# Optimization experiments

Measured on AMD Instinct MI355X. Metric: run time of the kernel, lower is better.

## Reference

```python
import jax, jax.numpy as jnp
import numpy as np

SNUM = 8           # number of select-PUF stages
PUF_LEN = 64       # arbiter PUF length -> phi dim = PUF_LEN + 1
BATCH = 262144     # number of challenge-response pairs
D = 2 ** SNUM      # 256 combinations


def _make_kron_tables():
    """Replicates the W/B kron construction from combineMPUF.__init__.
    Returns Wmat, Bmat of shape [SNUM, D]; row i is W[i]/B[i] (originally [1, D])."""
    tmpX = np.array([[1], [1]])
    Ws, Bs = [], []
    for i in range(SNUM):
        w = np.array([[-1], [1]])
        b = np.array([[1], [0]])
        for _ in range(i + 1, SNUM):
            w = np.kron(tmpX, w)
            b = np.kron(tmpX, b)
        for _ in range(i):
            w = np.kron(w, tmpX)
            b = np.kron(b, tmpX)
        Ws.append(w.T[0])
        Bs.append(b.T[0])
    return (jnp.asarray(np.stack(Ws), jnp.float32),
            jnp.asarray(np.stack(Bs), jnp.float32))


def setup_inputs() -> dict:
    key = jax.random.key(0)
    k_phi, k_ws, k_bs, k_wd, k_bd = jax.random.split(key, 5)
    F = PUF_LEN + 1
    scale = 1.0 / np.sqrt(F)  # ~ torch Linear init scale
    phi = jax.random.normal(k_phi, (BATCH, F), dtype=jnp.float32)
    W_S = jax.random.uniform(k_ws, (SNUM, F), jnp.float32, -scale, scale)
    b_S = jax.random.uniform(k_bs, (SNUM,), jnp.float32, -scale, scale)
    W_D = jax.random.uniform(k_wd, (D, F), jnp.float32, -scale, scale)
    b_D = jax.random.uniform(k_bd, (D,), jnp.float32, -scale, scale)
    Wmat, Bmat = _make_kron_tables()
    return {"phi": phi, "W_S": W_S, "b_S": b_S, "W_D": W_D, "b_D": b_D,
            "Wmat": Wmat, "Bmat": Bmat}


def reference(phi, W_S, b_S, W_D, b_D, Wmat, Bmat):
    # phi: [B, F]; W_S: [SNUM, F]; W_D: [D, F]; Wmat/Bmat: [SNUM, D]
    Sdelta = phi @ W_S.T + b_S            # [B, SNUM]
    Ddelta = phi @ W_D.T + b_D            # [B, D]
    Souts = jax.nn.sigmoid(Sdelta)        # [B, SNUM]
    Douts = jax.nn.sigmoid(Ddelta)        # [B, D]
    # sigmoid-gated outer-product chain: M = prod_i (s_i * w_i + b_i)
    M = jnp.ones_like(Douts)
    for i in range(SNUM):                 # small fixed structural loop
        M = M * (Souts[:, i:i + 1] * Wmat[i] + Bmat[i])
    ans = jnp.sum(Douts * M * 0.99999, axis=-1, keepdims=True)  # [B, 1]
    reliability_output = jnp.abs(Sdelta)  # [B, SNUM]
    return ans, reliability_output
```

## Files before the change

### kernel.cpp

```cpp
#include <hip/hip_runtime.h>

typedef float  f32x4  __attribute__((ext_vector_type(4)));
typedef float  f32x4a __attribute__((ext_vector_type(4), aligned(4)));
typedef __bf16 bf16x8 __attribute__((ext_vector_type(8)));
typedef short  short8 __attribute__((ext_vector_type(8)));

#define F      65
#define NTT    17
#define KS3    3
#define RPB    128
#define NEGL2E -1.4426950408889634f

__device__ __forceinline__ float fast_sigmoid(float x) {
  float e = __builtin_amdgcn_exp2f(NEGL2E * x);
  return __builtin_amdgcn_rcpf(1.0f + e);
}
__device__ __forceinline__ float sig_prescaled(float a) {
  return __builtin_amdgcn_rcpf(1.0f + __builtin_amdgcn_exp2f(a));
}
template<int CTRL>
__device__ __forceinline__ float dpp_mov(float v) {
  return __builtin_bit_cast(float,
    __builtin_amdgcn_update_dpp(0, __builtin_bit_cast(int, v), CTRL, 0xF, 0xF, true));
}
__device__ __forceinline__ float reduce16(float v) {
  v += dpp_mov<0xB1>(v);
  v += dpp_mov<0x4E>(v);
  v += dpp_mov<0x141>(v);
  v += dpp_mov<0x140>(v);
  return v;
}

__global__ void prep_w(const float* __restrict__ W_S, const float* __restrict__ b_S,
                       const float* __restrict__ W_D, const float* __restrict__ b_D,
                       unsigned short* __restrict__ wsb) {
  int b = blockIdx.x;
  int t = b / 3, s = b % 3;
  int l = threadIdx.x;
  int c = l & 15, q = l >> 4;
  short8 out;
#pragma unroll
  for (int j = 0; j < 8; ++j) {
    int k = 32 * s + 8 * q + j;
    float v = 0.0f;
    if (t < 16) {
      int n = 16 * t + c;
      if (k < F)       v = NEGL2E * W_D[n * F + k];
      else if (k == F) v = NEGL2E * b_D[n];
    } else if (c < 8) {
      if (k < F)       v = W_S[c * F + k];
      else if (k == F) v = b_S[c];
    }
    unsigned int u = __builtin_bit_cast(unsigned int, v);
    u += 0x7FFFu + ((u >> 16) & 1u);
    out[j] = (short)(u >> 16);
  }
  reinterpret_cast<short8*>(wsb)[b * 64 + l] = out;
}

__launch_bounds__(256, 6)
__global__ void mpuf_main(const float* __restrict__ phi,
                          const unsigned short* __restrict__ wsb,
                          float* __restrict__ out_ans,
                          float* __restrict__ out_rel) {
  __shared__ float soutv[RPB][12];
  __shared__ float mtT[16][132];
  __shared__ float mlT[16][132];
  __shared__ float relv[RPB][8];

  const int tid  = threadIdx.x;
  const int wave = tid >> 6;
  const int l    = tid & 63;
  const int c    = l & 15;
  const int q    = l >> 4;
  const int wrow = wave * 32;
  const int R0b  = wrow + q * 4;
  const int brow = blockIdx.x * RPB;
  const int tbase = blockIdx.x & 15;

  const float* prow0 = phi + (size_t)(brow + wrow + c) * F;
  const float* prow1 = prow0 + (size_t)16 * F;

  f32x4a f40[4], f41[4];
#pragma unroll
  for (int s = 0; s < 2; ++s) {
    f40[2 * s]     = *reinterpret_cast<const f32x4a*>(prow0 + 32 * s + 8 * q);
    f40[2 * s + 1] = *reinterpret_cast<const f32x4a*>(prow0 + 32 * s + 8 * q + 4);
    f41[2 * s]     = *reinterpret_cast<const f32x4a*>(prow1 + 32 * s + 8 * q);
    f41[2 * s + 1] = *reinterpret_cast<const f32x4a*>(prow1 + 32 * s + 8 * q + 4);
  }
  const float a640 = prow0[64];
  const float a641 = prow1[64];

  const short8* wsv = reinterpret_cast<const short8*>(wsb);
  short8 bcur[3], bnxt[3];
#pragma unroll
  for (int s = 0; s < 3; ++s) bcur[s] = wsv[(16 * KS3 + s) * 64 + l];
#pragma unroll
  for (int s = 0; s < 3; ++s) bnxt[s] = wsv[(tbase * KS3 + s) * 64 + l];

  bf16x8 af0[3], af1[3];
#pragma unroll
  for (int s = 0; s < 2; ++s) {
    bf16x8 v0, v1;
#pragma unroll
    for (int j = 0; j < 4; ++j) {
      v0[j]     = (__bf16)f40[s * 2][j];
      v0[j + 4] = (__bf16)f40[s * 2 + 1][j];
      v1[j]     = (__bf16)f41[s * 2][j];
      v1[j + 4] = (__bf16)f41[s * 2 + 1][j];
    }
    af0[s] = v0; af1[s] = v1;
  }
  {
    bf16x8 v0 = {}, v1 = {};
    if (q == 0) {
      v0[0] = (__bf16)a640; v0[1] = (__bf16)1.0f;
      v1[0] = (__bf16)a641; v1[1] = (__bf16)1.0f;
    }
    af0[2] = v0; af1[2] = v1;
  }

  f32x4 aS0 = {}, aS1 = {};
#pragma unroll
  for (int s = 0; s < KS3; ++s) {
    bf16x8 b = __builtin_bit_cast(bf16x8, bcur[s]);
    aS0 = __builtin_amdgcn_mfma_f32_16x16x32_bf16(af0[s], b, aS0, 0, 0, 0);
    aS1 = __builtin_amdgcn_mfma_f32_16x16x32_bf16(af1[s], b, aS1, 0, 0, 0);
  }
  if (c < 8) {
#pragma unroll
    for (int r = 0; r < 4; ++r) {
      const int R0 = R0b + r, R1 = R0 + 16;
      relv[R0][c]  = fabsf(aS0[r]);
      relv[R1][c]  = fabsf(aS1[r]);
      soutv[R0][c] = fast_sigmoid(aS0[r]);
      soutv[R1][c] = fast_sigmoid(aS1[r]);
    }
  }

  {
    const int row = l >> 1, half = l & 1;
    f32x4 v = *reinterpret_cast<const f32x4*>(&relv[wrow + row][half * 4]);
    *reinterpret_cast<f32x4*>(
        &out_rel[(size_t)(brow + wrow + row) * 8 + half * 4]) = v;
  }

#pragma unroll
  for (int rr = 0; rr < 8; ++rr) {
    const int R = wrow + (rr & 4) * 4 + q * 4 + (rr & 3);
    f32x4 s03 = *reinterpret_cast<const f32x4*>(&soutv[R][0]);
    f32x4 s47 = *reinterpret_cast<const f32x4*>(&soutv[R][4]);
    float m = 0.99999f;
    m *= (c & 1) ? s03[0] : 1.0f - s03[0];
    m *= (c & 2) ? s03[1] : 1.0f - s03[1];
    m *= (c & 4) ? s03[2] : 1.0f - s03[2];
    m *= (c & 8) ? s03[3] : 1.0f - s03[3];
    mlT[c][R] = m;
    float mt = (c & 1) ? s47[0] : 1.0f - s47[0];
    mt *= (c & 2) ? s47[1] : 1.0f - s47[1];
    mt *= (c & 4) ? s47[2] : 1.0f - s47[2];
    mt *= (c & 8) ? s47[3] : 1.0f - s47[3];
    mtT[c][R] = mt;
  }

  float ans0[4] = {0, 0, 0, 0}, ans1[4] = {0, 0, 0, 0};

#pragma unroll 1
  for (int tt = 0; tt < 16; ++tt) {
    const int t  = (tt + tbase) & 15;
    const int tn = (tt + 1 + tbase) & 15;
    short8 bt[3];
#pragma unroll
    for (int s = 0; s < 3; ++s) bt[s] = bnxt[s];
#pragma unroll
    for (int s = 0; s < 3; ++s)
      bnxt[s] = wsv[(tn * KS3 + s) * 64 + l];
    f32x4 w0 = *reinterpret_cast<const f32x4*>(&mtT[t][R0b]);
    f32x4 w1 = *reinterpret_cast<const f32x4*>(&mtT[t][R0b + 16]);
    f32x4 A0 = {}, A1 = {};
#pragma unroll
    for (int s = 0; s < KS3; ++s) {
      bf16x8 b = __builtin_bit_cast(bf16x8, bt[s]);
      A0 = __builtin_amdgcn_mfma_f32_16x16x32_bf16(af0[s], b, A0, 0, 0, 0);
      A1 = __builtin_amdgcn_mfma_f32_16x16x32_bf16(af1[s], b, A1, 0, 0, 0);
    }
#pragma unroll
    for (int r = 0; r < 4; ++r) {
      ans0[r] = fmaf(sig_prescaled(A0[r]), w0[r], ans0[r]);
      ans1[r] = fmaf(sig_prescaled(A1[r]), w1[r], ans1[r]);
    }
  }

  f32x4 ml0 = *reinterpret_cast<const f32x4*>(&mlT[c][R0b]);
  f32x4 ml1 = *reinterpret_cast<const f32x4*>(&mlT[c][R0b + 16]);
  f32x4 o0, o1;
#pragma unroll
  for (int r = 0; r < 4; ++r) {
    o0[r] = reduce16(ml0[r] * ans0[r]);
    o1[r] = reduce16(ml1[r] * ans1[r]);
  }
  if (c == 0) {
    *reinterpret_cast<f32x4*>(&out_ans[brow + wrow + q * 4])      = o0;
    *reinterpret_cast<f32x4*>(&out_ans[brow + wrow + 16 + q * 4]) = o1;
  }
}

extern "C" void kernel_launch(void* const* d_in, const int* in_sizes, int n_in,
                              void* d_out, int out_size, void* d_ws, size_t ws_size,
                              hipStream_t stream) {
  const float* phi = (const float*)d_in[0];
  const float* W_S = (const float*)d_in[1];
  const float* b_S = (const float*)d_in[2];
  const float* W_D = (const float*)d_in[3];
  const float* b_D = (const float*)d_in[4];
  const int rows = in_sizes[0] / F;
  unsigned short* wsb = (unsigned short*)d_ws;
  float* out_ans = (float*)d_out;
  float* out_rel = out_ans + rows;
  hipLaunchKernelGGL(prep_w, dim3(NTT * KS3), dim3(64), 0, stream,
                     W_S, b_S, W_D, b_D, wsb);
  hipLaunchKernelGGL(mpuf_main, dim3(rows / RPB), dim3(256), 0, stream,
                     phi, wsb, out_ans, out_rel);
}
```

Before: 37.25 us.

## Stage packed weights in LDS and double rows per block

Each 512-thread block now copies the whole packed bf16 weight table (about 52 KB) into shared memory once. The MFMA loops then read weight fragments from LDS instead of issuing per-wave global loads, and the per-block tile-rotation offset is dropped. The block size doubles to 256 rows. The low-half mask products stay in registers instead of going through a shared array, and the reliability staging buffer reuses the mtT storage. In exchange, the large LDS footprint and the extra barrier limit how many blocks fit per CU, and every block pays the cost of filling the table before any compute starts.

```diff
diff --git a/kernel.cpp b/kernel.cpp
--- a/kernel.cpp
+++ b/kernel.cpp
@@ -8,7 +8,8 @@
 #define F      65
 #define NTT    17
 #define KS3    3
-#define RPB    128
+#define RPB    256
+#define NCHUNK (NTT*KS3*64)
 #define NEGL2E -1.4426950408889634f
 
 __device__ __forceinline__ float fast_sigmoid(float x) {
@@ -58,15 +59,14 @@
   reinterpret_cast<short8*>(wsb)[b * 64 + l] = out;
 }
 
-__launch_bounds__(256, 6)
+__launch_bounds__(512, 4)
 __global__ void mpuf_main(const float* __restrict__ phi,
                           const unsigned short* __restrict__ wsb,
                           float* __restrict__ out_ans,
                           float* __restrict__ out_rel) {
-  __shared__ float soutv[RPB][12];
-  __shared__ float mtT[16][132];
-  __shared__ float mlT[16][132];
-  __shared__ float relv[RPB][8];
+  __shared__ short8 ldsB[NCHUNK];
+  __shared__ float  soutv[RPB][12];
+  __shared__ float  mtT[16][260];
 
   const int tid  = threadIdx.x;
   const int wave = tid >> 6;
@@ -76,7 +76,8 @@
   const int wrow = wave * 32;
   const int R0b  = wrow + q * 4;
   const int brow = blockIdx.x * RPB;
-  const int tbase = blockIdx.x & 15;
+
+  float* relbuf = &mtT[0][0];
 
   const float* prow0 = phi + (size_t)(brow + wrow + c) * F;
   const float* prow1 = prow0 + (size_t)16 * F;
@@ -93,11 +94,11 @@
   const float a641 = prow1[64];
 
   const short8* wsv = reinterpret_cast<const short8*>(wsb);
-  short8 bcur[3], bnxt[3];
-#pragma unroll
-  for (int s = 0; s < 3; ++s) bcur[s] = wsv[(16 * KS3 + s) * 64 + l];
-#pragma unroll
-  for (int s = 0; s < 3; ++s) bnxt[s] = wsv[(tbase * KS3 + s) * 64 + l];
+#pragma unroll
+  for (int i = 0; i < 7; ++i) {
+    int idx = tid + i * 512;
+    if (idx < NCHUNK) ldsB[idx] = wsv[idx];
+  }
 
   bf16x8 af0[3], af1[3];
 #pragma unroll
@@ -121,19 +122,26 @@
     af0[2] = v0; af1[2] = v1;
   }
 
+  __syncthreads();
+
   f32x4 aS0 = {}, aS1 = {};
 #pragma unroll
   for (int s = 0; s < KS3; ++s) {
-    bf16x8 b = __builtin_bit_cast(bf16x8, bcur[s]);
+    bf16x8 b = __builtin_bit_cast(bf16x8, ldsB[(16 * KS3 + s) * 64 + l]);
     aS0 = __builtin_amdgcn_mfma_f32_16x16x32_bf16(af0[s], b, aS0, 0, 0, 0);
     aS1 = __builtin_amdgcn_mfma_f32_16x16x32_bf16(af1[s], b, aS1, 0, 0, 0);
   }
+
+  short8 bnxt[3];
+#pragma unroll
+  for (int s = 0; s < 3; ++s) bnxt[s] = ldsB[s * 64 + l];
+
   if (c < 8) {
 #pragma unroll
     for (int r = 0; r < 4; ++r) {
       const int R0 = R0b + r, R1 = R0 + 16;
-      relv[R0][c]  = fabsf(aS0[r]);
-      relv[R1][c]  = fabsf(aS1[r]);
+      relbuf[R0 * 8 + c] = fabsf(aS0[r]);
+      relbuf[R1 * 8 + c] = fabsf(aS1[r]);
       soutv[R0][c] = fast_sigmoid(aS0[r]);
       soutv[R1][c] = fast_sigmoid(aS1[r]);
     }
@@ -141,11 +149,14 @@
 
   {
     const int row = l >> 1, half = l & 1;
-    f32x4 v = *reinterpret_cast<const f32x4*>(&relv[wrow + row][half * 4]);
+    f32x4 v = *reinterpret_cast<const f32x4*>(&relbuf[(wrow + row) * 8 + half * 4]);
     *reinterpret_cast<f32x4*>(
         &out_rel[(size_t)(brow + wrow + row) * 8 + half * 4]) = v;
   }
 
+  __syncthreads();
+
+  float Ml0[4], Ml1[4];
 #pragma unroll
   for (int rr = 0; rr < 8; ++rr) {
     const int R = wrow + (rr & 4) * 4 + q * 4 + (rr & 3);
@@ -156,7 +167,7 @@
     m *= (c & 2) ? s03[1] : 1.0f - s03[1];
     m *= (c & 4) ? s03[2] : 1.0f - s03[2];
     m *= (c & 8) ? s03[3] : 1.0f - s03[3];
-    mlT[c][R] = m;
+    if (rr < 4) Ml0[rr & 3] = m; else Ml1[rr & 3] = m;
     float mt = (c & 1) ? s47[0] : 1.0f - s47[0];
     mt *= (c & 2) ? s47[1] : 1.0f - s47[1];
     mt *= (c & 4) ? s47[2] : 1.0f - s47[2];
@@ -167,15 +178,14 @@
   float ans0[4] = {0, 0, 0, 0}, ans1[4] = {0, 0, 0, 0};
 
 #pragma unroll 1
-  for (int tt = 0; tt < 16; ++tt) {
-    const int t  = (tt + tbase) & 15;
-    const int tn = (tt + 1 + tbase) & 15;
+  for (int t = 0; t < 16; ++t) {
     short8 bt[3];
 #pragma unroll
     for (int s = 0; s < 3; ++s) bt[s] = bnxt[s];
+    const int tn = (t < 15) ? t + 1 : 15;
 #pragma unroll
     for (int s = 0; s < 3; ++s)
-      bnxt[s] = wsv[(tn * KS3 + s) * 64 + l];
+      bnxt[s] = ldsB[(tn * KS3 + s) * 64 + l];
     f32x4 w0 = *reinterpret_cast<const f32x4*>(&mtT[t][R0b]);
     f32x4 w1 = *reinterpret_cast<const f32x4*>(&mtT[t][R0b + 16]);
     f32x4 A0 = {}, A1 = {};
@@ -192,13 +202,11 @@
     }
   }
 
-  f32x4 ml0 = *reinterpret_cast<const f32x4*>(&mlT[c][R0b]);
-  f32x4 ml1 = *reinterpret_cast<const f32x4*>(&mlT[c][R0b + 16]);
   f32x4 o0, o1;
 #pragma unroll
   for (int r = 0; r < 4; ++r) {
-    o0[r] = reduce16(ml0[r] * ans0[r]);
-    o1[r] = reduce16(ml1[r] * ans1[r]);
+    o0[r] = reduce16(Ml0[r] * ans0[r]);
+    o1[r] = reduce16(Ml1[r] * ans1[r]);
   }
   if (c == 0) {
     *reinterpret_cast<f32x4*>(&out_ans[brow + wrow + q * 4])      = o0;
@@ -220,6 +228,6 @@
   float* out_rel = out_ans + rows;
   hipLaunchKernelGGL(prep_w, dim3(NTT * KS3), dim3(64), 0, stream,
                      W_S, b_S, W_D, b_D, wsb);
-  hipLaunchKernelGGL(mpuf_main, dim3(rows / RPB), dim3(256), 0, stream,
+  hipLaunchKernelGGL(mpuf_main, dim3(rows / RPB), dim3(512), 0, stream,
                      phi, wsb, out_ans, out_rel);
 }
```

New measurement: 36.92 us. About the same (-0.9%).
